# Performance work log

Hardware: AMD Instinct MI355X
Metric: run time of the kernel (lower is better)

The kernel has to match this reference:

```python
import jax, jax.numpy as jnp
import numpy as np

B, H, S = 2048, 1024, 128


def setup_inputs() -> dict:
    key = jax.random.key(0)
    ks = jax.random.split(key, 8)
    s = 0.05  # keep gates out of saturation, roughly 1/sqrt(H) init scale
    return {
        "hidden": jax.random.normal(ks[0], (1, B, H), jnp.float32) * s,
        "cell": jax.random.normal(ks[1], (1, B, H), jnp.float32) * s,
        "W_ih": jax.random.normal(ks[2], (4 * H, 1), jnp.float32) * s,
        "W_hh": jax.random.normal(ks[3], (4 * H, H), jnp.float32) * s,
        "b_ih": jax.random.normal(ks[4], (4 * H,), jnp.float32) * s,
        "b_hh": jax.random.normal(ks[5], (4 * H,), jnp.float32) * s,
        "W_fc": jax.random.normal(ks[6], (S, H), jnp.float32) * s,
        "b_fc": jax.random.normal(ks[7], (S,), jnp.float32) * s,
    }


def reference(hidden, cell, W_ih, W_hh, b_ih, b_hh, W_fc, b_fc):
    # prediction from per-step head fc_i fed back as next input.
    h0 = hidden[0]  # [B, H] (num_layers = 1)
    c0 = cell[0]
    b = b_ih + b_hh  # [4H]
    x0 = jnp.zeros((h0.shape[0], 1), h0.dtype)  # initial zero input [B, 1]

    def step(carry, fc_t):
        h, c, x = carry
        Wt, bt = fc_t  # Wt: [H], bt: scalar
        gates = x @ W_ih.T + h @ W_hh.T + b  # [B, 4H], torch gate order i,f,g,o
        i, f, g, o = jnp.split(gates, 4, axis=-1)
        c = jax.nn.sigmoid(f) * c + jax.nn.sigmoid(i) * jnp.tanh(g)
        h = jax.nn.sigmoid(o) * jnp.tanh(c)
        pred = h @ Wt + bt  # [B] (Linear(H,1) then squeeze)
        return (h, c, pred[:, None]), pred

    _, preds = jax.lax.scan(step, (h0, c0, x0), (W_fc, b_fc))  # preds: [S, B]
    return preds.T  # [B, S]
```

## Files before the change

### kernel.cpp

```cpp
#include <hip/hip_runtime.h>
#include <hip/hip_bf16.h>
#include <stdint.h>

#define B_SZ 2048
#define H_SZ 1024
#define S_SZ 128
#define G4   4096

typedef short short8 __attribute__((ext_vector_type(8)));
typedef float floatx4 __attribute__((ext_vector_type(4)));

#define AS1 __attribute__((address_space(1)))
#define AS3 __attribute__((address_space(3)))

__device__ ushort g_Wp[G4 * H_SZ];
__device__ ushort g_h[2][B_SZ * H_SZ];
__device__ float  g_c[B_SZ * H_SZ];
__device__ float  g_wih[G4];
__device__ float  g_bias[G4];

__device__ __forceinline__ float bf2f(ushort u) {
  return __uint_as_float(((unsigned)u) << 16);
}
__device__ __forceinline__ ushort f2bf(float f) {
  unsigned u = __float_as_uint(f);
  return (ushort)((u + 0x7FFFu + ((u >> 16) & 1u)) >> 16);
}
__device__ __forceinline__ float fsig(float x) { return 1.f / (1.f + __expf(-x)); }
__device__ __forceinline__ float ftanh(float x) { return 1.f - 2.f / (__expf(2.f * x) + 1.f); }

__device__ __forceinline__ void gload16(const void* g, void* l) {
  __builtin_amdgcn_global_load_lds((const AS1 void*)g, (AS3 void*)l, 16, 0, 0);
}


__global__ __launch_bounds__(256) void prep_wpack(const float* __restrict__ Whh) {
  const int gid = blockIdx.x * 256 + threadIdx.x;
  const int j   = gid >> 7;
  const int c8  = (gid & 127) << 3;
  const int gate = (j >> 4) & 3;
  const int h    = ((j >> 6) << 4) | (j & 15);
  const float* src = Whh + (size_t)(gate * H_SZ + h) * H_SZ + c8;
  floatx4 a = *(const floatx4*)src;
  floatx4 b = *(const floatx4*)(src + 4);
  short8 o;
#pragma unroll
  for (int i = 0; i < 4; ++i) o[i] = (short)f2bf(a[i]);
#pragma unroll
  for (int i = 0; i < 4; ++i) o[4 + i] = (short)f2bf(b[i]);
  *(short8*)&g_Wp[(size_t)j * H_SZ + c8] = o;
}

__global__ __launch_bounds__(256) void prep_misc(const float* __restrict__ Wih,
                                                 const float* __restrict__ bih,
                                                 const float* __restrict__ bhh) {
  const int j = blockIdx.x * 256 + threadIdx.x;
  const int gate = (j >> 4) & 3;
  const int h    = ((j >> 6) << 4) | (j & 15);
  const int jp   = gate * H_SZ + h;
  g_wih[j]  = Wih[jp];
  g_bias[j] = bih[jp] + bhh[jp];
}

__global__ __launch_bounds__(256) void prep_state(const float* __restrict__ hidden,
                                                  const float* __restrict__ cell) {
  const int gid = blockIdx.x * 256 + threadIdx.x;
  const int o8  = gid << 3;
  short8 o;
#pragma unroll
  for (int i = 0; i < 8; ++i) o[i] = (short)f2bf(hidden[o8 + i]);
  *(short8*)&g_h[0][o8] = o;
  floatx4 c0 = *(const floatx4*)&cell[o8];
  floatx4 c1 = *(const floatx4*)&cell[o8 + 4];
  *(floatx4*)&g_c[o8]     = c0;
  *(floatx4*)&g_c[o8 + 4] = c1;
}

__global__ __launch_bounds__(256, 2)
void lstm_step(int t, int p,
               const float* __restrict__ wfc_prev,
               const float* __restrict__ bfc_prev,
               float* __restrict__ out) {
  __shared__ ushort Alds[128 * 32];
  __shared__ ushort Blds[128 * 32];
  __shared__ float wfc_s[32];
  __shared__ float xred[256];
  __shared__ float xbuf[128];

  const ushort* __restrict__ hin = g_h[p];
  ushort* __restrict__ hout      = g_h[p ^ 1];

  const int tid  = threadIdx.x;
  const int lane = tid & 63;
  const int wid  = tid >> 6;
  const int jt   = blockIdx.x;
  const int brow = blockIdx.y << 7;
  const int jcol = jt << 7;

  const int wr = wid >> 1, wc = wid & 1;
  const int lr = lane & 15, lk = lane >> 4;

  floatx4 acc[4][4];
#pragma unroll
  for (int m = 0; m < 4; ++m)
#pragma unroll
    for (int n = 0; n < 4; ++n) acc[m][n] = {0.f, 0.f, 0.f, 0.f};

  float xacc = 0.f;
  const int srow  = lane >> 2;
  const int skq   = (lane & 3) * 8;
  const int prow  = tid & 127;
  const int phalf = tid >> 7;

  for (int kk = 0; kk < 32; ++kk) {
    const int kbase = kk * 32 + skq;
    gload16(hin + (size_t)(brow + wid * 16 + srow) * H_SZ + kbase, &Alds[wid * 512]);
    gload16(hin + (size_t)(brow + (wid + 4) * 16 + srow) * H_SZ + kbase, &Alds[(wid + 4) * 512]);
    gload16(g_Wp + (size_t)(jcol + wid * 16 + srow) * H_SZ + kbase, &Blds[wid * 512]);
    gload16(g_Wp + (size_t)(jcol + (wid + 4) * 16 + srow) * H_SZ + kbase, &Blds[(wid + 4) * 512]);
    if (t > 0 && tid < 32) wfc_s[tid] = wfc_prev[kk * 32 + tid];
    __syncthreads();

    short8 a[4], b[4];
#pragma unroll
    for (int m = 0; m < 4; ++m)
      a[m] = *(const short8*)&Alds[(wr * 64 + m * 16 + lr) * 32 + lk * 8];
#pragma unroll
    for (int n = 0; n < 4; ++n)
      b[n] = *(const short8*)&Blds[(wc * 64 + n * 16 + lr) * 32 + lk * 8];
#pragma unroll
    for (int m = 0; m < 4; ++m)
#pragma unroll
      for (int n = 0; n < 4; ++n)
        acc[m][n] = __builtin_amdgcn_mfma_f32_16x16x32_bf16(a[m], b[n], acc[m][n], 0, 0, 0);

    if (t > 0) {
      short8 v0 = *(const short8*)&Alds[prow * 32 + phalf * 16];
      short8 v1 = *(const short8*)&Alds[prow * 32 + phalf * 16 + 8];
#pragma unroll
      for (int i = 0; i < 8; ++i) xacc += bf2f((ushort)v0[i]) * wfc_s[phalf * 16 + i];
#pragma unroll
      for (int i = 0; i < 8; ++i) xacc += bf2f((ushort)v1[i]) * wfc_s[phalf * 16 + 8 + i];
    }
    __syncthreads();
  }

  if (t > 0) {
    xred[tid] = xacc;
    __syncthreads();
    if (tid < 128) {
      float pr = xred[tid] + xred[tid + 128] + bfc_prev[0];
      xbuf[tid] = pr;
      if (jt == 0) out[(size_t)(brow + tid) * S_SZ + (t - 1)] = pr;
    }
    __syncthreads();
  }

  const int hcol = ((jt * 2 + wc) << 4) + lr;
  float wih[4], bb[4];
#pragma unroll
  for (int n = 0; n < 4; ++n) {
    const int col = jcol + wc * 64 + n * 16 + lr;
    wih[n] = g_wih[col];
    bb[n]  = g_bias[col];
  }
#pragma unroll
  for (int m = 0; m < 4; ++m) {
    const int rbase = wr * 64 + m * 16 + lk * 4;
#pragma unroll
    for (int r = 0; r < 4; ++r) {
      const int row_l = rbase + r;
      const float xv  = (t > 0) ? xbuf[row_l] : 0.f;
      float gi = acc[m][0][r] + xv * wih[0] + bb[0];
      float gf = acc[m][1][r] + xv * wih[1] + bb[1];
      float gg = acc[m][2][r] + xv * wih[2] + bb[2];
      float go = acc[m][3][r] + xv * wih[3] + bb[3];
      const size_t idx = (size_t)(brow + row_l) * H_SZ + hcol;
      float cc = g_c[idx];
      float cn = fsig(gf) * cc + fsig(gi) * ftanh(gg);
      g_c[idx] = cn;
      hout[idx] = f2bf(fsig(go) * ftanh(cn));
    }
  }
}

__global__ __launch_bounds__(256)
void pred_last(const float* __restrict__ wfc, const float* __restrict__ bfc,
               float* __restrict__ out) {
  const int tid = threadIdx.x;
  const int l16 = tid & 15;
  const int row = blockIdx.x * 16 + (tid >> 4);
  const ushort* hp = g_h[0] + (size_t)row * H_SZ;
  float acc = 0.f;
#pragma unroll
  for (int i = 0; i < 8; ++i) {
    const int k0 = i * 128 + l16 * 8;
    short8 v = *(const short8*)&hp[k0];
#pragma unroll
    for (int j = 0; j < 8; ++j) acc += bf2f((ushort)v[j]) * wfc[k0 + j];
  }
#pragma unroll
  for (int o = 8; o; o >>= 1) acc += __shfl_xor(acc, o, 64);
  if (l16 == 0) out[(size_t)row * S_SZ + (S_SZ - 1)] = acc + bfc[0];
}

extern "C" void kernel_launch(void* const* d_in, const int* in_sizes, int n_in,
                              void* d_out, int out_size, void* d_ws, size_t ws_size,
                              hipStream_t stream) {
  const float* hidden = (const float*)d_in[0];
  const float* cell   = (const float*)d_in[1];
  const float* W_ih   = (const float*)d_in[2];
  const float* W_hh   = (const float*)d_in[3];
  const float* b_ih   = (const float*)d_in[4];
  const float* b_hh   = (const float*)d_in[5];
  const float* W_fc   = (const float*)d_in[6];
  const float* b_fc   = (const float*)d_in[7];
  float* out = (float*)d_out;

  prep_wpack<<<2048, 256, 0, stream>>>(W_hh);
  prep_misc<<<16, 256, 0, stream>>>(W_ih, b_ih, b_hh);
  prep_state<<<1024, 256, 0, stream>>>(hidden, cell);

  dim3 grid(32, 16);
  for (int t = 0; t < S_SZ; ++t) {
    const int tp = (t > 0) ? (t - 1) : 0;
    lstm_step<<<grid, 256, 0, stream>>>(t, t & 1, W_fc + (size_t)tp * H_SZ,
                                        b_fc + tp, out);
  }
  pred_last<<<128, 256, 0, stream>>>(W_fc + (size_t)(S_SZ - 1) * H_SZ,
                                     b_fc + (S_SZ - 1), out);
}
```

Baseline: 5.855 ms.

## Double-buffer LDS with BK=64, XOR-swizzle layout, fuse prediction into step epilogue

Raises the K tile from 32 to 64 and double-buffers the LDS tiles, so each global-to-LDS load overlaps MFMA work on the other buffer and fewer barriers run per step. The bf16 h and packed W_hh are stored with an XOR swizzle on the column index to cut LDS bank conflicts. The per-step scalar prediction now comes from the freshly computed h in the epilogue: each block writes a partial dot product to a global scratch array, and the next step sums the 32 partials instead of redoing the dot product in the K loop. The trade-offs are more LDS per block (which may lower occupancy) and an extra cross-block partial buffer.

```diff
diff --git a/kernel.cpp b/kernel.cpp
--- a/kernel.cpp
+++ b/kernel.cpp
@@ -6,6 +6,8 @@
 #define H_SZ 1024
 #define S_SZ 128
 #define G4   4096
+#define BK   64
+#define NKK  (H_SZ / BK)
 
 typedef short short8 __attribute__((ext_vector_type(8)));
 typedef float floatx4 __attribute__((ext_vector_type(4)));
@@ -18,6 +20,7 @@
 __device__ float  g_c[B_SZ * H_SZ];
 __device__ float  g_wih[G4];
 __device__ float  g_bias[G4];
+__device__ float  g_pp[2][32][B_SZ];
 
 __device__ __forceinline__ float bf2f(ushort u) {
   return __uint_as_float(((unsigned)u) << 16);
@@ -37,10 +40,10 @@
 __global__ __launch_bounds__(256) void prep_wpack(const float* __restrict__ Whh) {
   const int gid = blockIdx.x * 256 + threadIdx.x;
   const int j   = gid >> 7;
-  const int c8  = (gid & 127) << 3;
+  const int k8  = (gid & 127) << 3;
   const int gate = (j >> 4) & 3;
   const int h    = ((j >> 6) << 4) | (j & 15);
-  const float* src = Whh + (size_t)(gate * H_SZ + h) * H_SZ + c8;
+  const float* src = Whh + (size_t)(gate * H_SZ + h) * H_SZ + k8;
   floatx4 a = *(const floatx4*)src;
   floatx4 b = *(const floatx4*)(src + 4);
   short8 o;
@@ -48,7 +51,7 @@
   for (int i = 0; i < 4; ++i) o[i] = (short)f2bf(a[i]);
 #pragma unroll
   for (int i = 0; i < 4; ++i) o[4 + i] = (short)f2bf(b[i]);
-  *(short8*)&g_Wp[(size_t)j * H_SZ + c8] = o;
+  *(short8*)&g_Wp[(size_t)j * H_SZ + (k8 ^ ((j & 7) << 3))] = o;
 }
 
 __global__ __launch_bounds__(256) void prep_misc(const float* __restrict__ Wih,
@@ -65,27 +68,24 @@
 __global__ __launch_bounds__(256) void prep_state(const float* __restrict__ hidden,
                                                   const float* __restrict__ cell) {
   const int gid = blockIdx.x * 256 + threadIdx.x;
-  const int o8  = gid << 3;
+  const int row = gid >> 7;
+  const int k8  = (gid & 127) << 3;
+  const size_t src = (size_t)row * H_SZ + k8;
   short8 o;
 #pragma unroll
-  for (int i = 0; i < 8; ++i) o[i] = (short)f2bf(hidden[o8 + i]);
-  *(short8*)&g_h[0][o8] = o;
-  floatx4 c0 = *(const floatx4*)&cell[o8];
-  floatx4 c1 = *(const floatx4*)&cell[o8 + 4];
-  *(floatx4*)&g_c[o8]     = c0;
-  *(floatx4*)&g_c[o8 + 4] = c1;
+  for (int i = 0; i < 8; ++i) o[i] = (short)f2bf(hidden[src + i]);
+  *(short8*)&g_h[0][(size_t)row * H_SZ + (k8 ^ ((row & 7) << 3))] = o;
+  floatx4 c0 = *(const floatx4*)&cell[src];
+  floatx4 c1 = *(const floatx4*)&cell[src + 4];
+  *(floatx4*)&g_c[src]     = c0;
+  *(floatx4*)&g_c[src + 4] = c1;
 }
 
 __global__ __launch_bounds__(256, 2)
-void lstm_step(int t, int p,
-               const float* __restrict__ wfc_prev,
-               const float* __restrict__ bfc_prev,
-               float* __restrict__ out) {
-  __shared__ ushort Alds[128 * 32];
-  __shared__ ushort Blds[128 * 32];
-  __shared__ float wfc_s[32];
-  __shared__ float xred[256];
-  __shared__ float xbuf[128];
+void lstm_step(int t, int p, const float* __restrict__ Wfc,
+               const float* __restrict__ bfc, float* __restrict__ out) {
+  __shared__ ushort Al[2][128 * BK];
+  __shared__ ushort Bl[2][128 * BK];
 
   const ushort* __restrict__ hin = g_h[p];
   ushort* __restrict__ hout      = g_h[p ^ 1];
@@ -96,9 +96,18 @@
   const int jt   = blockIdx.x;
   const int brow = blockIdx.y << 7;
   const int jcol = jt << 7;
-
   const int wr = wid >> 1, wc = wid & 1;
   const int lr = lane & 15, lk = lane >> 4;
+  const int xorv = (lr & 7) << 3;
+
+  const int srow = lane >> 3;
+  const int scol = (lane & 7) << 3;
+  const size_t arb = (size_t)(brow + wid * 32 + srow) * H_SZ + scol;
+  const size_t brb = (size_t)(jcol + wid * 32 + srow) * H_SZ + scol;
+  ushort* const ad0 = &Al[0][wid * 32 * BK];
+  ushort* const ad1 = &Al[1][wid * 32 * BK];
+  ushort* const bd0 = &Bl[0][wid * 32 * BK];
+  ushort* const bd1 = &Bl[1][wid * 32 * BK];
 
   floatx4 acc[4][4];
 #pragma unroll
@@ -106,57 +115,66 @@
 #pragma unroll
     for (int n = 0; n < 4; ++n) acc[m][n] = {0.f, 0.f, 0.f, 0.f};
 
-  float xacc = 0.f;
-  const int srow  = lane >> 2;
-  const int skq   = (lane & 3) * 8;
-  const int prow  = tid & 127;
-  const int phalf = tid >> 7;
-
-  for (int kk = 0; kk < 32; ++kk) {
-    const int kbase = kk * 32 + skq;
-    gload16(hin + (size_t)(brow + wid * 16 + srow) * H_SZ + kbase, &Alds[wid * 512]);
-    gload16(hin + (size_t)(brow + (wid + 4) * 16 + srow) * H_SZ + kbase, &Alds[(wid + 4) * 512]);
-    gload16(g_Wp + (size_t)(jcol + wid * 16 + srow) * H_SZ + kbase, &Blds[wid * 512]);
-    gload16(g_Wp + (size_t)(jcol + (wid + 4) * 16 + srow) * H_SZ + kbase, &Blds[(wid + 4) * 512]);
-    if (t > 0 && tid < 32) wfc_s[tid] = wfc_prev[kk * 32 + tid];
+  int aoff[4], boff[4];
+#pragma unroll
+  for (int m = 0; m < 4; ++m) aoff[m] = (wr * 64 + m * 16 + lr) * BK;
+#pragma unroll
+  for (int n = 0; n < 4; ++n) boff[n] = (wc * 64 + n * 16 + lr) * BK;
+  const int c0 = (lk * 8) ^ xorv;
+  const int c1 = (32 + lk * 8) ^ xorv;
+
+#define STAGE(AD, BD, KO)                                                   \
+  {                                                                         \
+    const int ko_ = (KO) * BK;                                              \
+    _Pragma("unroll") for (int i = 0; i < 4; ++i) {                         \
+      gload16(hin + arb + (size_t)i * 8 * H_SZ + ko_, AD + i * 8 * BK);     \
+      gload16(g_Wp + brb + (size_t)i * 8 * H_SZ + ko_, BD + i * 8 * BK);    \
+    }                                                                       \
+  }
+
+#define COMPUTE(AC, BC)                                                     \
+  {                                                                         \
+    short8 a[4], b[4];                                                      \
+    _Pragma("unroll") for (int k2 = 0; k2 < 2; ++k2) {                      \
+      const int cc_ = k2 ? c1 : c0;                                         \
+      _Pragma("unroll") for (int m = 0; m < 4; ++m)                         \
+          a[m] = *(const short8*)&(AC)[aoff[m] + cc_];                      \
+      _Pragma("unroll") for (int n = 0; n < 4; ++n)                         \
+          b[n] = *(const short8*)&(BC)[boff[n] + cc_];                      \
+      _Pragma("unroll") for (int m = 0; m < 4; ++m)                         \
+          _Pragma("unroll") for (int n = 0; n < 4; ++n)                     \
+              acc[m][n] = __builtin_amdgcn_mfma_f32_16x16x32_bf16(          \
+                  a[m], b[n], acc[m][n], 0, 0, 0);                          \
+    }                                                                       \
+  }
+
+  STAGE(ad0, bd0, 0);
+  __syncthreads();
+
+  for (int kk = 0; kk < NKK; kk += 2) {
+    STAGE(ad1, bd1, kk + 1);
+    COMPUTE(Al[0], Bl[0]);
     __syncthreads();
-
-    short8 a[4], b[4];
-#pragma unroll
-    for (int m = 0; m < 4; ++m)
-      a[m] = *(const short8*)&Alds[(wr * 64 + m * 16 + lr) * 32 + lk * 8];
-#pragma unroll
-    for (int n = 0; n < 4; ++n)
-      b[n] = *(const short8*)&Blds[(wc * 64 + n * 16 + lr) * 32 + lk * 8];
-#pragma unroll
-    for (int m = 0; m < 4; ++m)
-#pragma unroll
-      for (int n = 0; n < 4; ++n)
-        acc[m][n] = __builtin_amdgcn_mfma_f32_16x16x32_bf16(a[m], b[n], acc[m][n], 0, 0, 0);
-
-    if (t > 0) {
-      short8 v0 = *(const short8*)&Alds[prow * 32 + phalf * 16];
-      short8 v1 = *(const short8*)&Alds[prow * 32 + phalf * 16 + 8];
-#pragma unroll
-      for (int i = 0; i < 8; ++i) xacc += bf2f((ushort)v0[i]) * wfc_s[phalf * 16 + i];
-#pragma unroll
-      for (int i = 0; i < 8; ++i) xacc += bf2f((ushort)v1[i]) * wfc_s[phalf * 16 + 8 + i];
-    }
+    if (kk + 2 < NKK) STAGE(ad0, bd0, kk + 2);
+    COMPUTE(Al[1], Bl[1]);
     __syncthreads();
   }
 
-  if (t > 0) {
-    xred[tid] = xacc;
-    __syncthreads();
-    if (tid < 128) {
-      float pr = xred[tid] + xred[tid + 128] + bfc_prev[0];
-      xbuf[tid] = pr;
-      if (jt == 0) out[(size_t)(brow + tid) * S_SZ + (t - 1)] = pr;
-    }
-    __syncthreads();
-  }
+  float* predp = (float*)&Al[0][0];
+  float* xbuf  = (float*)&Bl[0][0];
+
+  if (t > 0 && tid < 128) {
+    float s = 0.f;
+#pragma unroll
+    for (int j = 0; j < 32; ++j) s += g_pp[(t - 1) & 1][j][brow + tid];
+    s += bfc[t - 1];
+    xbuf[tid] = s;
+    if (jt == 0) out[(size_t)(brow + tid) * S_SZ + (t - 1)] = s;
+  }
+  __syncthreads();
 
   const int hcol = ((jt * 2 + wc) << 4) + lr;
+  const float wfc_l = Wfc[(size_t)t * H_SZ + hcol];
   float wih[4], bb[4];
 #pragma unroll
   for (int n = 0; n < 4; ++n) {
@@ -164,44 +182,45 @@
     wih[n] = g_wih[col];
     bb[n]  = g_bias[col];
   }
+
 #pragma unroll
   for (int m = 0; m < 4; ++m) {
-    const int rbase = wr * 64 + m * 16 + lk * 4;
 #pragma unroll
     for (int r = 0; r < 4; ++r) {
-      const int row_l = rbase + r;
-      const float xv  = (t > 0) ? xbuf[row_l] : 0.f;
+      const int row_l = wr * 64 + m * 16 + lk * 4 + r;
+      const float xv = (t > 0) ? xbuf[row_l] : 0.f;
       float gi = acc[m][0][r] + xv * wih[0] + bb[0];
       float gf = acc[m][1][r] + xv * wih[1] + bb[1];
       float gg = acc[m][2][r] + xv * wih[2] + bb[2];
       float go = acc[m][3][r] + xv * wih[3] + bb[3];
-      const size_t idx = (size_t)(brow + row_l) * H_SZ + hcol;
-      float cc = g_c[idx];
+      const int row = brow + row_l;
+      const size_t cidx = (size_t)row * H_SZ + hcol;
+      float cc = g_c[cidx];
       float cn = fsig(gf) * cc + fsig(gi) * ftanh(gg);
-      g_c[idx] = cn;
-      hout[idx] = f2bf(fsig(go) * ftanh(cn));
+      g_c[cidx] = cn;
+      float hv = fsig(go) * ftanh(cn);
+      hout[(size_t)row * H_SZ + (hcol ^ ((row_l & 7) << 3))] = f2bf(hv);
+      float pp = hv * wfc_l;
+      pp += __shfl_xor(pp, 1);
+      pp += __shfl_xor(pp, 2);
+      pp += __shfl_xor(pp, 4);
+      pp += __shfl_xor(pp, 8);
+      if (lr == 0) predp[wc * 128 + row_l] = pp;
     }
   }
+  __syncthreads();
+  if (tid < 128) g_pp[t & 1][jt][brow + tid] = predp[tid] + predp[128 + tid];
+#undef STAGE
+#undef COMPUTE
 }
 
 __global__ __launch_bounds__(256)
-void pred_last(const float* __restrict__ wfc, const float* __restrict__ bfc,
-               float* __restrict__ out) {
-  const int tid = threadIdx.x;
-  const int l16 = tid & 15;
-  const int row = blockIdx.x * 16 + (tid >> 4);
-  const ushort* hp = g_h[0] + (size_t)row * H_SZ;
-  float acc = 0.f;
-#pragma unroll
-  for (int i = 0; i < 8; ++i) {
-    const int k0 = i * 128 + l16 * 8;
-    short8 v = *(const short8*)&hp[k0];
-#pragma unroll
-    for (int j = 0; j < 8; ++j) acc += bf2f((ushort)v[j]) * wfc[k0 + j];
-  }
-#pragma unroll
-  for (int o = 8; o; o >>= 1) acc += __shfl_xor(acc, o, 64);
-  if (l16 == 0) out[(size_t)row * S_SZ + (S_SZ - 1)] = acc + bfc[0];
+void pred_last(const float* __restrict__ bfc, float* __restrict__ out) {
+  const int row = blockIdx.x * 256 + threadIdx.x;
+  float s = 0.f;
+#pragma unroll
+  for (int j = 0; j < 32; ++j) s += g_pp[1][j][row];
+  out[(size_t)row * S_SZ + (S_SZ - 1)] = s + bfc[S_SZ - 1];
 }
 
 extern "C" void kernel_launch(void* const* d_in, const int* in_sizes, int n_in,
@@ -223,10 +242,7 @@
 
   dim3 grid(32, 16);
   for (int t = 0; t < S_SZ; ++t) {
-    const int tp = (t > 0) ? (t - 1) : 0;
-    lstm_step<<<grid, 256, 0, stream>>>(t, t & 1, W_fc + (size_t)tp * H_SZ,
-                                        b_fc + tp, out);
-  }
-  pred_last<<<128, 256, 0, stream>>>(W_fc + (size_t)(S_SZ - 1) * H_SZ,
-                                     b_fc + (S_SZ - 1), out);
-}
+    lstm_step<<<grid, 256, 0, stream>>>(t, t & 1, W_fc, b_fc, out);
+  }
+  pred_last<<<8, 256, 0, stream>>>(b_fc, out);
+}
```

New measurement: 4.941 ms. 1.18x faster.
